# Kernel tuning notes

Measured on AMD Instinct MI355X. Metric: run time of the kernel, lower is better.

Reference implementation:

```python
import jax, jax.numpy as jnp
import numpy as np
from jax import lax

KS = 21      # ksize
SCALE = 4    # downscale stride


def _conv(x, w, b=None, padding='SAME'):
    # x: NCHW, w: OIHW
    y = lax.conv_general_dilated(x, w, (1, 1), padding,
                                 dimension_numbers=('NCHW', 'OIHW', 'NCHW'))
    if b is not None:
        y = y + b[None, :, None, None]
    return y


def _deg_kernel_net(z, conv0_w, conv0_b, res_w1, res_b1, res_w2, res_b2, last_w, last_b):
    # conv3x3 -> nb EDSR ResBlocks (conv-relu-conv + residual) -> conv1x1 to ksize^2
    h = _conv(z, conv0_w, conv0_b)
    for i in range(res_w1.shape[0]):  # fixed small layer count
        r = _conv(jax.nn.relu(_conv(h, res_w1[i], res_b1[i])), res_w2[i], res_b2[i])
        h = h + r
    return _conv(h, last_w, last_b)  # (B, ksize^2, H', W')


def setup_inputs() -> dict:
    key = jax.random.key(0)
    ks = jax.random.split(key, 10)
    B, C, H, W = 8, 3, 256, 256
    nf, nb, k2 = 64, 8, KS * KS
    s = 0.05  # keep activations tame through 8 residual blocks
    return {
        'x': jax.random.normal(ks[0], (B, C, H, W), jnp.float32),
        'z': jax.random.normal(ks[1], (B, C, H // SCALE, W // SCALE), jnp.float32),
        'conv0_w': jax.random.normal(ks[2], (nf, C, 3, 3), jnp.float32) * s,
        'conv0_b': jax.random.normal(ks[3], (nf,), jnp.float32) * s,
        'res_w1': jax.random.normal(ks[4], (nb, nf, nf, 3, 3), jnp.float32) * s,
        'res_b1': jax.random.normal(ks[5], (nb, nf), jnp.float32) * s,
        'res_w2': jax.random.normal(ks[6], (nb, nf, nf, 3, 3), jnp.float32) * s,
        'res_b2': jax.random.normal(ks[7], (nb, nf), jnp.float32) * s,
        'last_w': jax.random.normal(ks[8], (k2, nf, 1, 1), jnp.float32) * s,
        'last_b': jax.random.normal(ks[9], (k2,), jnp.float32) * s,
    }


def reference(x, z, conv0_w, conv0_b, res_w1, res_b1, res_w2, res_b2, last_w, last_b):
    B, C, H, W = x.shape
    hz, wz = z.shape[2], z.shape[3]
    k2 = KS * KS

    # spatially-varying kernel, normalized over the ksize^2 taps
    kernel = _deg_kernel_net(z, conv0_w, conv0_b, res_w1, res_b1,
                             res_w2, res_b2, last_w, last_b)
    kernel = kernel.reshape(B, 1, k2, hz, wz)
    kernel = kernel / (kernel.sum(axis=2, keepdims=True) + 1e-8)

    # reflection pad then unfold (im2col) with stride = scale
    p = KS // 2
    xp = jnp.pad(x.reshape(B * C, 1, H, W), ((0, 0), (0, 0), (p, p), (p, p)),
                 mode='reflect')
    patches = lax.conv_general_dilated_patches(
        xp, (KS, KS), (SCALE, SCALE), 'VALID',
        dimension_numbers=('NCHW', 'OIHW', 'NCHW'))  # (B*C, k2, hz, wz)
    patches = patches.reshape(B, C, k2, hz, wz)

    out = (patches * kernel).sum(axis=2)  # (B, C, hz, wz)
    return out, kernel.reshape(B, k2, hz, wz)
```

## Files before the change

kernel.cpp:

```cpp
#include <hip/hip_runtime.h>


#define NB 8
#define NF 64
#define SP 4096
#define PS 66
#define PS2 4356
#define K2 441
#define K2P 448
#define RES_WSTRIDE (64*64*9)
#define WF_RES 36864
#define WF_C0  1792
#define WTA_N  28672

typedef double vdbl4 __attribute__((ext_vector_type(4)));

#define T_AI 0
#define T_AK 64
#define T_BK 128
#define T_BJ 192
#define T_DI 256
#define T_DJ 512

__global__ void probe_mfma(double* __restrict__ probe)
{
    int l = threadIdx.x;
    vdbl4 z = {0.0, 0.0, 0.0, 0.0};
    vdbl4 r1 = __builtin_amdgcn_mfma_f64_16x16x4f64((double)l, 1.0, z, 0, 0, 0);
    vdbl4 r2 = __builtin_amdgcn_mfma_f64_16x16x4f64(1.0, (double)l, z, 0, 0, 0);
#pragma unroll
    for (int r = 0; r < 4; ++r) {
        probe[r * 64 + l]       = r1[r];
        probe[256 + r * 64 + l] = r2[r];
    }
}

__global__ void decode_probe(const double* __restrict__ probe, int* __restrict__ tabs)
{
    int t = threadIdx.x;
    const double* d1 = probe;
    const double* d2 = probe + 256;
    bool fA = ((((int)d1[0]) & 3) == 0);
    bool fB = ((((int)d2[0]) & 3) == 0);
    int v1 = (int)d1[t], v2 = (int)d2[t];
    tabs[T_DI + t] = fA ? (v1 - 96) >> 2 : (v1 - 6) >> 4;
    tabs[T_DJ + t] = fB ? (v2 - 96) >> 2 : (v2 - 6) >> 4;
    if (t < 64) {
        tabs[T_AI + t] = fA ? (t & 15) : (t >> 2);
        tabs[T_AK + t] = fA ? (t >> 4) : (t & 3);
        tabs[T_BK + t] = fB ? (t >> 4) : (t & 3);
        tabs[T_BJ + t] = fB ? (t & 15) : (t >> 2);
    }
}

__global__ void prep_zpad(const float* __restrict__ z, double* __restrict__ zp)
{
    int i = blockIdx.x * blockDim.x + threadIdx.x;
    if (i >= NB * 3 * SP) return;
    int bc = i >> 12, p = i & 4095, y = p >> 6, x = p & 63;
    zp[(size_t)(bc * PS + y + 1) * PS + x + 1] = (double)z[i];
}

__global__ void prep_convw_frag(const float* __restrict__ src, double* __restrict__ dst,
                                const int* __restrict__ tabs,
                                int CIN, int nlayer, int wstride)
{
    int i = blockIdx.x * blockDim.x + threadIdx.x;
    int NS = (CIN * 9 + 3) / 4;
    int M  = NS * 256;
    if (i >= nlayer * M) return;
    int li  = i / M;
    int rem = i - li * M;
    int t   = rem >> 8;
    int j   = rem & 255;
    int mt  = j >> 6;
    int l   = j & 63;
    int kg  = t * 4 + tabs[T_AK + l];
    int oc  = mt * 16 + tabs[T_AI + l];
    int c   = kg / 9;
    int tap = kg - c * 9;
    dst[i] = (kg < CIN * 9) ? (double)src[li * wstride + (oc * CIN + c) * 9 + tap] : 0.0;
}

__global__ void prep_bias_frag(const float* __restrict__ src, double* __restrict__ dst,
                               const int* __restrict__ tabs, int nlayer)
{
    int i = blockIdx.x * blockDim.x + threadIdx.x;
    if (i >= nlayer * 1024) return;
    int li  = i >> 10;
    int j   = i & 1023;
    int mtr = j >> 6;
    int l   = j & 63;
    int mt  = mtr >> 2, r = mtr & 3;
    dst[i] = (double)src[li * 64 + mt * 16 + tabs[T_DI + r * 64 + l]];
}

__global__ void prep_lastwa(const float* __restrict__ lw, const float* __restrict__ lb,
                            const int* __restrict__ tabs,
                            double* __restrict__ wta, double* __restrict__ lbp)
{
    int i = blockIdx.x * blockDim.x + threadIdx.x;
    if (i < WTA_N) {
        int kk = i / (28 * 64);
        int rem = i - kk * (28 * 64);
        int mt = rem >> 6;
        int l  = rem & 63;
        int c  = kk * 4 + tabs[T_AK + l];
        int T  = mt * 16 + tabs[T_AI + l];
        wta[i] = (T < K2) ? (double)lw[T * 64 + c] : 0.0;
    }
    if (i < K2P) lbp[i] = (i < K2) ? (double)lb[i] : 0.0;
}

__global__ void prep_wsum(const float* __restrict__ lw, const float* __restrict__ lb,
                          double* __restrict__ wsum)
{
    int c = threadIdx.x;
    if (c < 64) {
        double s = 0.0;
        for (int t = 0; t < K2; ++t) s += (double)lw[t * 64 + c];
        wsum[c] = s;
    }
    if (c == 64) {
        double s = 0.0;
        for (int t = 0; t < K2; ++t) s += (double)lb[t];
        wsum[64] = s;
    }
}

template<int CIN, bool RELU, bool RESADD>
__global__ __launch_bounds__(256, 2)
void conv3x3_mfma(const double* __restrict__ in, const double* __restrict__ WF,
                  const double* __restrict__ BF, const int* __restrict__ tabs,
                  const double* __restrict__ res, double* __restrict__ out)
{
    constexpr int KT = CIN * 9;
    constexpr int NS = (KT + 3) / 4;
    constexpr int G  = (NS + 8) / 9;

    const int bid = blockIdx.x;
    const int b   = bid & 7;
    const int y0  = bid >> 3;
    const int tid = threadIdx.x;
    const int w   = tid >> 6;
    const int l   = tid & 63;
    const int mi  = w >> 1, ni = w & 1;
    const int mt0 = mi * 2, nt0 = ni * 2;

    const int kB = tabs[T_BK + l];
    const int jB = tabs[T_BJ + l];

    int offp[9];
#pragma unroll
    for (int s = 0; s < 9; ++s) {
        int kg  = s * 4 + kB;
        int off = 0;
        if (KT >= 36 || kg < KT) {
            int c   = kg / 9;
            int tap = kg - c * 9;
            int dy  = tap / 3, dx = tap - dy * 3;
            off = c * PS2 + dy * PS + dx;
        }
        offp[s] = off + jB + nt0 * 16;
    }

    const double* bbase = in + (size_t)b * CIN * PS2 + (size_t)y0 * PS;

    vdbl4 acc[2][2];
#pragma unroll
    for (int mt = 0; mt < 2; ++mt)
#pragma unroll
        for (int r = 0; r < 4; ++r) {
            double bv = BF[((mt0 + mt) * 4 + r) * 64 + l];
            acc[mt][0][r] = bv;
            acc[mt][1][r] = bv;
        }

    double aS[3][2], bS[3][2];
    auto ldA = [&](int t, int slot) {
        const double* p = WF + (size_t)t * 256 + l;
        aS[slot][0] = p[mt0 * 64];
        aS[slot][1] = p[(mt0 + 1) * 64];
    };
    auto ldB = [&](size_t cg, int s, int slot) {
        const double* p = bbase + cg + offp[s];
        bS[slot][0] = p[0];
        bS[slot][1] = p[16];
    };
    auto step = [&](int slot) {
        acc[0][0] = __builtin_amdgcn_mfma_f64_16x16x4f64(aS[slot][0], bS[slot][0], acc[0][0], 0, 0, 0);
        acc[0][1] = __builtin_amdgcn_mfma_f64_16x16x4f64(aS[slot][0], bS[slot][1], acc[0][1], 0, 0, 0);
        acc[1][0] = __builtin_amdgcn_mfma_f64_16x16x4f64(aS[slot][1], bS[slot][0], acc[1][0], 0, 0, 0);
        acc[1][1] = __builtin_amdgcn_mfma_f64_16x16x4f64(aS[slot][1], bS[slot][1], acc[1][1], 0, 0, 0);
    };

    ldA(0, 0); ldB(0, 0, 0);
    ldA(1, 1); ldB(0, 1, 1);

    for (int g = 0; g < G; ++g) {
        const size_t cg = (size_t)g * 4 * PS2;
#pragma unroll
        for (int s = 0; s < 9; ++s) {
            const int t = g * 9 + s;
            if (KT % 36 != 0 && t >= NS) break;
            const int tp = t + 2;
            if (tp < NS) {
                const int    ps  = (s + 2 < 9) ? s + 2 : s - 7;
                const size_t pcg = (s + 2 < 9) ? cg : cg + 4 * PS2;
                ldA(tp, (s + 2) % 3);
                ldB(pcg, ps, (s + 2) % 3);
            }
            step(s % 3);
        }
    }

    int iD[4], jD[4];
#pragma unroll
    for (int r = 0; r < 4; ++r) {
        iD[r] = tabs[T_DI + r * 64 + l];
        jD[r] = tabs[T_DJ + r * 64 + l];
    }
#pragma unroll
    for (int mt = 0; mt < 2; ++mt)
#pragma unroll
        for (int nt = 0; nt < 2; ++nt)
#pragma unroll
            for (int r = 0; r < 4; ++r) {
                int oc = (mt0 + mt) * 16 + iD[r];
                int x  = (nt0 + nt) * 16 + jD[r];
                size_t idx = (size_t)(b * NF + oc) * PS2 + (size_t)(y0 + 1) * PS + x + 1;
                double val = acc[mt][nt][r];
                if (RELU)   val = fmax(val, 0.0);
                if (RESADD) val += res[idx];
                out[idx] = val;
            }
}

__global__ __launch_bounds__(256, 2)
void lastconv_mfma(const double* __restrict__ hp, const double* __restrict__ wta,
                   const double* __restrict__ lbp, const int* __restrict__ tabs,
                   float* __restrict__ kraw)
{
    const int bid = blockIdx.x;
    const int b   = bid / 224;
    const int rem = bid - b * 224;
    const int tg  = rem >> 5;
    const int pc  = rem & 31;
    const int tid = threadIdx.x;
    const int w   = tid >> 6;
    const int l   = tid & 63;
    const int mt  = tg * 4 + w;

    const int kB = tabs[T_BK + l];
    const int jB = tabs[T_BJ + l];
    int iD[4], jD[4];
#pragma unroll
    for (int r = 0; r < 4; ++r) {
        iD[r] = tabs[T_DI + r * 64 + l];
        jD[r] = tabs[T_DJ + r * 64 + l];
    }

    double avs[16];
#pragma unroll
    for (int kk = 0; kk < 16; ++kk)
        avs[kk] = wta[((size_t)kk * 28 + mt) * 64 + l];

    double bias[4];
#pragma unroll
    for (int r = 0; r < 4; ++r)
        bias[r] = lbp[mt * 16 + iD[r]];

    const double* hb = hp + (size_t)b * NF * PS2;
    float* kb = kraw + (size_t)b * K2 * SP;

    for (int q = 0; q < 2; ++q) {
        const int P0  = pc * 128 + q * 64;
        const int row = P0 >> 6;
        const double* hrow = hb + (size_t)(row + 1) * PS + 1 + jB;

        vdbl4 acc[4];
#pragma unroll
        for (int j = 0; j < 4; ++j)
#pragma unroll
            for (int r = 0; r < 4; ++r)
                acc[j][r] = bias[r];

        double bc[4], bn[4];
#pragma unroll
        for (int j = 0; j < 4; ++j)
            bc[j] = hrow[(size_t)kB * PS2 + j * 16];

        for (int kk = 0; kk < 16; ++kk) {
            if (kk < 15) {
                const double* np = hrow + (size_t)((kk + 1) * 4 + kB) * PS2;
#pragma unroll
                for (int j = 0; j < 4; ++j) bn[j] = np[j * 16];
            }
#pragma unroll
            for (int j = 0; j < 4; ++j)
                acc[j] = __builtin_amdgcn_mfma_f64_16x16x4f64(avs[kk], bc[j], acc[j], 0, 0, 0);
#pragma unroll
            for (int j = 0; j < 4; ++j) bc[j] = bn[j];
        }

#pragma unroll
        for (int r = 0; r < 4; ++r) {
            int T = mt * 16 + iD[r];
            if (T < K2) {
                float* p = kb + (size_t)T * SP + P0;
                p[jD[r]]      = (float)acc[0][r];
                p[16 + jD[r]] = (float)acc[1][r];
                p[32 + jD[r]] = (float)acc[2][r];
                p[48 + jD[r]] = (float)acc[3][r];
            }
        }
    }
}

__global__ __launch_bounds__(256)
void sums_kernel(const double* __restrict__ hp, const double* __restrict__ wsum,
                 double* __restrict__ sums)
{
    int i = blockIdx.x * 256 + threadIdx.x;
    int b = i >> 12, p = i & 4095;
    int y = p >> 6, x = p & 63;
    const double* hb = hp + (size_t)b * NF * PS2 + (size_t)(y + 1) * PS + 1 + x;
    double s = wsum[64];
    for (int c = 0; c < 64; ++c) s += hb[(size_t)c * PS2] * wsum[c];
    sums[b * SP + p] = s;
}

__global__ __launch_bounds__(256)
void apply_kernel(const float* __restrict__ x, const double* __restrict__ sums,
                  float* __restrict__ kout, float* __restrict__ out)
{
    const int bid  = blockIdx.x;
    const int g    = bid & 3;
    const int tile = (bid >> 2) & 15;
    const int b    = bid >> 6;
    const int i0   = (tile >> 2) << 4;
    const int j0   = (tile & 3) << 4;
    const int tid  = threadIdx.x;
    const int ti   = tid >> 4, tj = tid & 15;

    __shared__ float s_x[3][81][84];

    for (int e = tid; e < 3 * 81 * 84; e += 256) {
        int c   = e / 6804;
        int rem = e - c * 6804;
        int u   = rem / 84;
        int v   = rem - u * 84;
        int gr  = i0 * 4 + u - 10;
        int gc  = j0 * 4 + v - 10;
        gr = gr < 0 ? -gr : (gr > 255 ? 510 - gr : gr);
        gc = gc < 0 ? -gc : (gc > 255 ? 510 - gc : gc);
        int vp = (v & 3) * 21 + (v >> 2);
        s_x[c][u][vp] = x[((b * 3 + c) * 256 + gr) * 256 + gc];
    }
    __syncthreads();

    const int p = (i0 + ti) * 64 + (j0 + tj);
    const double inv = 1.0 / (sums[b * SP + p] + 1e-8);

    float o0 = 0.f, o1 = 0.f, o2 = 0.f;
    const int t0 = g * 111;
    const int t1 = (t0 + 111 < K2) ? t0 + 111 : K2;
    for (int t = t0; t < t1; ++t) {
        int ty = t / 21, tx = t - ty * 21;
        float* kp = &kout[(size_t)(b * K2 + t) * SP + p];
        float k  = *kp;
        float kn = (float)((double)k * inv);
        *kp = kn;
        int u  = ti * 4 + ty;
        int vp = (tx & 3) * 21 + tj + (tx >> 2);
        o0 = fmaf(s_x[0][u][vp], kn, o0);
        o1 = fmaf(s_x[1][u][vp], kn, o1);
        o2 = fmaf(s_x[2][u][vp], kn, o2);
    }
    atomicAdd(&out[(b * 3 + 0) * SP + p], o0);
    atomicAdd(&out[(b * 3 + 1) * SP + p], o1);
    atomicAdd(&out[(b * 3 + 2) * SP + p], o2);
}

extern "C" void kernel_launch(void* const* d_in, const int* in_sizes, int n_in,
                              void* d_out, int out_size, void* d_ws, size_t ws_size,
                              hipStream_t stream)
{
    (void)in_sizes; (void)n_in; (void)out_size; (void)ws_size;

    const float* x = (const float*)d_in[0];
    const float* z = (const float*)d_in[1];

    float* out  = (float*)d_out;
    float* kout = (float*)d_out + NB * 3 * SP;

    double* wd    = (double*)d_ws;
    double* probe = wd;
    int*    tabs  = (int*)(wd + 512);
    double* wf0   = wd + 1024;
    double* wf1   = wf0 + WF_C0;
    double* wf2   = wf1 + 8 * WF_RES;
    double* bf0   = wf2 + 8 * WF_RES;
    double* bf1   = bf0 + 1024;
    double* bf2   = bf1 + 8 * 1024;
    double* wta   = bf2 + 8 * 1024;
    double* lbp   = wta + WTA_N;
    double* wsum  = lbp + K2P;
    double* zp    = wsum + 72;
    double* hp    = zp + NB * 3 * PS2;
    double* tp    = hp + NB * NF * PS2;
    double* sums  = tp;

    hipMemsetAsync(zp, 0, (size_t)NB * 3 * PS2 * sizeof(double), stream);
    hipMemsetAsync(hp, 0, (size_t)NB * NF * PS2 * sizeof(double), stream);
    hipMemsetAsync(tp, 0, (size_t)NB * NF * PS2 * sizeof(double), stream);
    hipMemsetAsync(out, 0, NB * 3 * SP * sizeof(float), stream);

    probe_mfma<<<1, 64, 0, stream>>>(probe);
    decode_probe<<<1, 256, 0, stream>>>(probe, tabs);

    prep_zpad<<<(NB * 3 * SP + 255) / 256, 256, 0, stream>>>(z, zp);
    prep_convw_frag<<<(WF_C0 + 255) / 256, 256, 0, stream>>>(
        (const float*)d_in[2], wf0, tabs, 3, 1, 0);
    prep_convw_frag<<<(8 * WF_RES + 255) / 256, 256, 0, stream>>>(
        (const float*)d_in[4], wf1, tabs, 64, 8, RES_WSTRIDE);
    prep_convw_frag<<<(8 * WF_RES + 255) / 256, 256, 0, stream>>>(
        (const float*)d_in[6], wf2, tabs, 64, 8, RES_WSTRIDE);
    prep_bias_frag<<<(1024 + 255) / 256, 256, 0, stream>>>(
        (const float*)d_in[3], bf0, tabs, 1);
    prep_bias_frag<<<(8 * 1024 + 255) / 256, 256, 0, stream>>>(
        (const float*)d_in[5], bf1, tabs, 8);
    prep_bias_frag<<<(8 * 1024 + 255) / 256, 256, 0, stream>>>(
        (const float*)d_in[7], bf2, tabs, 8);
    prep_lastwa<<<(WTA_N + 255) / 256, 256, 0, stream>>>(
        (const float*)d_in[8], (const float*)d_in[9], tabs, wta, lbp);
    prep_wsum<<<1, 128, 0, stream>>>(
        (const float*)d_in[8], (const float*)d_in[9], wsum);

    conv3x3_mfma<3,  false, false><<<512, 256, 0, stream>>>(zp, wf0, bf0, tabs, nullptr, hp);
    for (int i = 0; i < 8; ++i) {
        conv3x3_mfma<64, true,  false><<<512, 256, 0, stream>>>(
            hp, wf1 + i * WF_RES, bf1 + i * 1024, tabs, nullptr, tp);
        conv3x3_mfma<64, false, true ><<<512, 256, 0, stream>>>(
            tp, wf2 + i * WF_RES, bf2 + i * 1024, tabs, hp, hp);
    }
    sums_kernel<<<128, 256, 0, stream>>>(hp, wsum, sums);
    lastconv_mfma<<<1792, 256, 0, stream>>>(hp, wta, lbp, tabs, kout);
    apply_kernel<<<512, 256, 0, stream>>>(x, sums, kout, out);
}
```

Measured before the change: 912.2 us.

## Fuse kernel normalization into last conv and deepen conv3x3 prefetch pipeline

The inverse kernel sum is now computed in the sums kernel and applied inside the last 1x1 conv epilogue. The apply kernel therefore only reads the normalized kernel instead of reading, rescaling and writing it back, which removes a full read-modify-write pass over the large kernel tensor. The conv3x3 main loop is also restructured into 36-step supergroups with a 4-slot register ring and prefetch distance 3 instead of 2. This should hide more load latency but uses more registers.

```diff
diff --git a/kernel.cpp b/kernel.cpp
--- a/kernel.cpp
+++ b/kernel.cpp
@@ -134,9 +134,10 @@
                   const double* __restrict__ BF, const int* __restrict__ tabs,
                   const double* __restrict__ res, double* __restrict__ out)
 {
-    constexpr int KT = CIN * 9;
-    constexpr int NS = (KT + 3) / 4;
-    constexpr int G  = (NS + 8) / 9;
+    constexpr int KT   = CIN * 9;
+    constexpr int NS   = (KT + 3) / 4;
+    constexpr int NSG  = NS / 36;
+    constexpr int TAIL = NS % 36;
 
     const int bid = blockIdx.x;
     const int b   = bid & 7;
@@ -176,14 +177,14 @@
             acc[mt][1][r] = bv;
         }
 
-    double aS[3][2], bS[3][2];
+    double aS[4][2], bS[4][2];
     auto ldA = [&](int t, int slot) {
         const double* p = WF + (size_t)t * 256 + l;
         aS[slot][0] = p[mt0 * 64];
         aS[slot][1] = p[(mt0 + 1) * 64];
     };
-    auto ldB = [&](size_t cg, int s, int slot) {
-        const double* p = bbase + cg + offp[s];
+    auto ldB = [&](const double* base, int idx9, int cg4, int slot) {
+        const double* p = base + (size_t)cg4 * 4 * PS2 + offp[idx9];
         bS[slot][0] = p[0];
         bS[slot][1] = p[16];
     };
@@ -194,23 +195,37 @@
         acc[1][1] = __builtin_amdgcn_mfma_f64_16x16x4f64(aS[slot][1], bS[slot][1], acc[1][1], 0, 0, 0);
     };
 
-    ldA(0, 0); ldB(0, 0, 0);
-    ldA(1, 1); ldB(0, 1, 1);
-
-    for (int g = 0; g < G; ++g) {
-        const size_t cg = (size_t)g * 4 * PS2;
-#pragma unroll
-        for (int s = 0; s < 9; ++s) {
-            const int t = g * 9 + s;
-            if (KT % 36 != 0 && t >= NS) break;
-            const int tp = t + 2;
-            if (tp < NS) {
-                const int    ps  = (s + 2 < 9) ? s + 2 : s - 7;
-                const size_t pcg = (s + 2 < 9) ? cg : cg + 4 * PS2;
-                ldA(tp, (s + 2) % 3);
-                ldB(pcg, ps, (s + 2) % 3);
+    ldA(0, 0); ldB(bbase, 0, 0, 0);
+    ldA(1, 1); ldB(bbase, 1, 0, 1);
+    ldA(2, 2); ldB(bbase, 2, 0, 2);
+
+    for (int sg = 0; sg < NSG; ++sg) {
+        const double* sgb = bbase + (size_t)sg * 16 * PS2;
+        const int t0 = sg * 36;
+#pragma unroll
+        for (int s = 0; s < 36; ++s) {
+            const int sp = s + 3;
+            if (sp < 36) {
+                ldA(t0 + sp, sp & 3);
+                ldB(sgb, sp % 9, sp / 9, sp & 3);
+            } else if (sg + 1 < NSG || (TAIL > 0 && sp - 36 < TAIL)) {
+                ldA(t0 + sp, sp & 3);
+                ldB(sgb + (size_t)16 * PS2, sp - 36, 0, sp & 3);
             }
-            step(s % 3);
+            step(s & 3);
+        }
+    }
+    if (TAIL > 0) {
+        const double* tb = bbase + (size_t)NSG * 16 * PS2;
+        const int t0 = NSG * 36;
+#pragma unroll
+        for (int s = 0; s < TAIL; ++s) {
+            const int sp = s + 3;
+            if (sp < TAIL) {
+                ldA(t0 + sp, sp & 3);
+                ldB(tb, sp, 0, sp & 3);
+            }
+            step(s & 3);
         }
     }
 
@@ -239,7 +254,7 @@
 __global__ __launch_bounds__(256, 2)
 void lastconv_mfma(const double* __restrict__ hp, const double* __restrict__ wta,
                    const double* __restrict__ lbp, const int* __restrict__ tabs,
-                   float* __restrict__ kraw)
+                   const double* __restrict__ inv_sums, float* __restrict__ kraw)
 {
     const int bid = blockIdx.x;
     const int b   = bid / 224;
@@ -278,6 +293,14 @@
         const int row = P0 >> 6;
         const double* hrow = hb + (size_t)(row + 1) * PS + 1 + jB;
 
+        const double* isrow = inv_sums + (size_t)b * SP + P0;
+        double isv[4][4];
+#pragma unroll
+        for (int j = 0; j < 4; ++j)
+#pragma unroll
+            for (int r = 0; r < 4; ++r)
+                isv[j][r] = isrow[j * 16 + jD[r]];
+
         vdbl4 acc[4];
 #pragma unroll
         for (int j = 0; j < 4; ++j)
@@ -308,10 +331,10 @@
             int T = mt * 16 + iD[r];
             if (T < K2) {
                 float* p = kb + (size_t)T * SP + P0;
-                p[jD[r]]      = (float)acc[0][r];
-                p[16 + jD[r]] = (float)acc[1][r];
-                p[32 + jD[r]] = (float)acc[2][r];
-                p[48 + jD[r]] = (float)acc[3][r];
+                p[jD[r]]      = (float)(acc[0][r] * isv[0][r]);
+                p[16 + jD[r]] = (float)(acc[1][r] * isv[1][r]);
+                p[32 + jD[r]] = (float)(acc[2][r] * isv[2][r]);
+                p[48 + jD[r]] = (float)(acc[3][r] * isv[3][r]);
             }
         }
     }
@@ -319,7 +342,7 @@
 
 __global__ __launch_bounds__(256)
 void sums_kernel(const double* __restrict__ hp, const double* __restrict__ wsum,
-                 double* __restrict__ sums)
+                 double* __restrict__ inv_sums)
 {
     int i = blockIdx.x * 256 + threadIdx.x;
     int b = i >> 12, p = i & 4095;
@@ -327,12 +350,12 @@
     const double* hb = hp + (size_t)b * NF * PS2 + (size_t)(y + 1) * PS + 1 + x;
     double s = wsum[64];
     for (int c = 0; c < 64; ++c) s += hb[(size_t)c * PS2] * wsum[c];
-    sums[b * SP + p] = s;
+    inv_sums[b * SP + p] = 1.0 / (s + 1e-8);
 }
 
 __global__ __launch_bounds__(256)
-void apply_kernel(const float* __restrict__ x, const double* __restrict__ sums,
-                  float* __restrict__ kout, float* __restrict__ out)
+void apply_kernel(const float* __restrict__ x, const float* __restrict__ kout,
+                  float* __restrict__ out)
 {
     const int bid  = blockIdx.x;
     const int g    = bid & 3;
@@ -360,17 +383,13 @@
     __syncthreads();
 
     const int p = (i0 + ti) * 64 + (j0 + tj);
-    const double inv = 1.0 / (sums[b * SP + p] + 1e-8);
 
     float o0 = 0.f, o1 = 0.f, o2 = 0.f;
     const int t0 = g * 111;
     const int t1 = (t0 + 111 < K2) ? t0 + 111 : K2;
     for (int t = t0; t < t1; ++t) {
         int ty = t / 21, tx = t - ty * 21;
-        float* kp = &kout[(size_t)(b * K2 + t) * SP + p];
-        float k  = *kp;
-        float kn = (float)((double)k * inv);
-        *kp = kn;
+        float kn = kout[(size_t)(b * K2 + t) * SP + p];
         int u  = ti * 4 + ty;
         int vp = (tx & 3) * 21 + tj + (tx >> 2);
         o0 = fmaf(s_x[0][u][vp], kn, o0);
@@ -445,6 +464,6 @@
             tp, wf2 + i * WF_RES, bf2 + i * 1024, tabs, hp, hp);
     }
     sums_kernel<<<128, 256, 0, stream>>>(hp, wsum, sums);
-    lastconv_mfma<<<1792, 256, 0, stream>>>(hp, wta, lbp, tabs, kout);
-    apply_kernel<<<512, 256, 0, stream>>>(x, sums, kout, out);
-}
+    lastconv_mfma<<<1792, 256, 0, stream>>>(hp, wta, lbp, tabs, sums, kout);
+    apply_kernel<<<512, 256, 0, stream>>>(x, kout, out);
+}
```

New measurement: 998.1 us. 9.4% more time.
